# Optimization experiments

Measured on AMD Instinct MI355X. Metric: run time of the kernel, lower is better.

## Reference

```python
import jax, jax.numpy as jnp
import numpy as np

B, T, HH, WW, D, NH, MLPD, KH, KW = 2, 16, 24, 24, 128, 4, 512, 5, 5
T_ = T + 1
HW = HH * WW
SIZE = KH * KW
PH, PW = KH // 2, KW // 2


def _ln(x, w, b):
    m = x.mean(-1, keepdims=True)
    v = ((x - m) ** 2).mean(-1, keepdims=True)
    return (x - m) / jnp.sqrt(v + 1e-5) * w + b


def _mha(q, kv, mask, Wq, bq, Wk, bk, Wv, bv, Wo, bo):
    # q: (N, Lq, D), kv: (N, Lk, D), mask: (N, Lq|1, Lk) True = masked
    N, Lq, Dm = q.shape
    dh = Dm // NH
    qh = (q @ Wq + bq).reshape(N, Lq, NH, dh).transpose(0, 2, 1, 3)
    kh = (kv @ Wk + bk).reshape(N, -1, NH, dh).transpose(0, 2, 1, 3)
    vh = (kv @ Wv + bv).reshape(N, -1, NH, dh).transpose(0, 2, 1, 3)
    scores = jnp.einsum('nhqd,nhkd->nhqk', qh, kh) * (1.0 / np.sqrt(dh))
    logits = jnp.where(mask[:, None, :, :], -1e9, scores)
    attn = jax.nn.softmax(logits, axis=-1)
    out = jnp.einsum('nhqk,nhkd->nhqd', attn, vh).transpose(0, 2, 1, 3).reshape(N, Lq, Dm)
    return out @ Wo + bo, logits


def _unfold_patches(x):
    # x: (N, H, W, D) -> (N, H, W, SIZE, D), kernel positions row-major (matches F.unfold)
    xp = jnp.pad(x, ((0, 0), (PH, PH), (PW, PW), (0, 0)))
    return jnp.stack([xp[:, i:i + HH, j:j + WW, :] for i in range(KH) for j in range(KW)], axis=3)


def setup_inputs() -> dict:
    key = jax.random.key(0)
    ks = iter(jax.random.split(key, 48))
    w = lambda *s: jax.random.normal(next(ks), s, jnp.float32) * 0.02
    inp = {
        'query': jax.random.normal(next(ks), (B, T_, HW, D), jnp.float32),
        'spatial_mask': jnp.zeros((1,), bool),  # ignored by the module
        'temporal_mask': jnp.zeros((B * HW, T_, T_), bool),
        'ln_s_w': jnp.ones((D,), jnp.float32), 'ln_s_b': jnp.zeros((D,), jnp.float32),
        'sWq': w(D, D), 'sbq': jnp.zeros((D,), jnp.float32),
        'sWk': w(D, D), 'sbk': jnp.zeros((D,), jnp.float32),
        'sWv': w(D, D), 'sbv': jnp.zeros((D,), jnp.float32),
        'sWo': w(D, D), 'sbo': jnp.zeros((D,), jnp.float32),
        'ln_t_w': jnp.ones((D,), jnp.float32), 'ln_t_b': jnp.zeros((D,), jnp.float32),
        'tWq': w(D, D), 'tbq': jnp.zeros((D,), jnp.float32),
        'tWk': w(D, D), 'tbk': jnp.zeros((D,), jnp.float32),
        'tWv': w(D, D), 'tbv': jnp.zeros((D,), jnp.float32),
        'tWo': w(D, D), 'tbo': jnp.zeros((D,), jnp.float32),
        'ln_m_w': jnp.ones((D,), jnp.float32), 'ln_m_b': jnp.zeros((D,), jnp.float32),
        'mW1': w(D, MLPD), 'mb1': jnp.zeros((MLPD,), jnp.float32),
        'mW2': w(MLPD, D), 'mb2': jnp.zeros((D,), jnp.float32),
    }
    return inp


def reference(query, spatial_mask, temporal_mask, ln_s_w, ln_s_b, sWq, sbq, sWk, sbk, sWv, sbv, sWo, sbo,
              ln_t_w, ln_t_b, tWq, tbq, tWk, tbk, tWv, tbv, tWo, tbo, ln_m_w, ln_m_b, mW1, mb1, mW2, mb2):
    # ---- spatial branch (local window attention + global CLS key) ----
    visual = query[:, 1:].reshape(B * T, HH, WW, D)
    neigh = _unfold_patches(visual).reshape(B * T * HW, SIZE, D)
    vis = visual.reshape(B * T * HW, 1, D)
    cls = query[:, 0].mean(axis=1, keepdims=True)              # (B,1,D)
    cls_rep = jnp.tile(cls, (T * HW, 1, 1))                    # faithful to torch .repeat ordering
    kv = jnp.concatenate([cls_rep, neigh], axis=1)             # (N, SIZE+1, D)
    # padding mask: True where neighbor falls outside the frame (faithful: CLS zero-col appended LAST)
    valid = jnp.pad(jnp.ones((HH, WW), bool), ((PH, PH), (PW, PW)))
    mpat = jnp.stack([valid[i:i + HH, j:j + WW] for i in range(KH) for j in range(KW)], axis=2).reshape(HW, SIZE)
    smask = jnp.concatenate([~mpat, jnp.zeros((HW, 1), bool)], axis=1)           # (HW, SIZE+1)
    smask = jnp.broadcast_to(smask[None], (B * T, HW, SIZE + 1)).reshape(B * T * HW, 1, SIZE + 1)
    out, _ = _mha(_ln(vis, ln_s_w, ln_s_b), _ln(kv, ln_s_w, ln_s_b), smask,
                  sWq, sbq, sWk, sbk, sWv, sbv, sWo, sbo)
    x = out + vis
    x = jnp.concatenate([query[:, 0:1], x.reshape(B, T, HW, D)], axis=1)  # (B, T_, HW, D)
    # ---- temporal branch ----
    xt = x.transpose(0, 2, 1, 3).reshape(B * HW, T_, D)
    xn = _ln(xt, ln_t_w, ln_t_b)
    x_, logits = _mha(xn, xn, temporal_mask, tWq, tbq, tWk, tbk, tWv, tbv, tWo, tbo)
    xt = x_ + xt
    x = xt.reshape(B, HW, T_, D).transpose(0, 2, 1, 3)
    x = x.at[:, 0].set(x[:, 0:1].mean(axis=2))                 # average CLS across spatial locations
    logits = logits.reshape(B, HW, NH, T_, T_)
    # ---- MLP ----
    h = _ln(x, ln_m_w, ln_m_b)
    h = jax.nn.gelu(h @ mW1 + mb1, approximate=False) @ mW2 + mb2
    x = h + x
    return x, logits
```

## Files before the change

### kernel.cpp

```cpp
#include <hip/hip_runtime.h>
#include <math.h>

#define BB    2
#define TT    16
#define TP    17
#define HH_   24
#define WW_   24
#define HWW   576
#define DD    128
#define NHH   4
#define MLPD_ 512
#define NPIX  18432
#define NTOK  19584
#define SCALE 0.17677669529663688f
#define OUT0_SIZE 2506752

typedef unsigned short u16;
typedef __bf16 bf16x8 __attribute__((ext_vector_type(8)));
typedef float f32x4 __attribute__((ext_vector_type(4)));

__device__ __forceinline__ u16 f2b(float f) {
  unsigned u = __float_as_uint(f);
  u += 0x7FFFu + ((u >> 16) & 1u);
  return (u16)(u >> 16);
}
__device__ __forceinline__ float blo(unsigned u) { return __uint_as_float(u << 16); }
__device__ __forceinline__ float bhi(unsigned u) { return __uint_as_float(u & 0xFFFF0000u); }
__device__ __forceinline__ float b2f(u16 u) { return __uint_as_float((unsigned)u << 16); }

__device__ __forceinline__ float dot8p(uint4 a, uint4 b) {
  float s = blo(a.x) * blo(b.x) + bhi(a.x) * bhi(b.x);
  s += blo(a.y) * blo(b.y) + bhi(a.y) * bhi(b.y);
  s += blo(a.z) * blo(b.z) + bhi(a.z) * bhi(b.z);
  s += blo(a.w) * blo(b.w) + bhi(a.w) * bhi(b.w);
  return s;
}
__device__ __forceinline__ float getp(const float4* P, int j) {
  float4 v = P[j >> 2];
  switch (j & 3) { case 0: return v.x; case 1: return v.y; case 2: return v.z; default: return v.w; }
}
__device__ __forceinline__ void gld_lds16(const void* g, void* l) {
  __builtin_amdgcn_global_load_lds(
      (const __attribute__((address_space(1))) void*)g,
      (__attribute__((address_space(3))) void*)l, 16, 0, 0);
}
__device__ __forceinline__ float fgelu(float x) {
  float u = x * (0.7978845608028654f + 0.03567740814f * x * x);
  u = fminf(fmaxf(u, -15.f), 15.f);
  float e = __expf(2.0f * u);
  return x * e / (e + 1.0f);
}

#define QLN8_BODY(SP, Q8, LNW, LNB, EMIT)                                        \
  {                                                                              \
    const float4* s4_ = (const float4*)(SP) + (Q8) * 4;                          \
    float4 xv_[4];                                                               \
    float sum_ = 0.f, sq_ = 0.f;                                                 \
    _Pragma("unroll")                                                            \
    for (int i_ = 0; i_ < 4; i_++) {                                             \
      float4 a_ = s4_[i_]; xv_[i_] = a_;                                         \
      sum_ += (a_.x + a_.y) + (a_.z + a_.w);                                     \
      sq_  += a_.x * a_.x + a_.y * a_.y + a_.z * a_.z + a_.w * a_.w;             \
    }                                                                            \
    sum_ += __shfl_xor(sum_, 1, 8); sum_ += __shfl_xor(sum_, 2, 8);              \
    sum_ += __shfl_xor(sum_, 4, 8);                                              \
    sq_  += __shfl_xor(sq_, 1, 8);  sq_  += __shfl_xor(sq_, 2, 8);               \
    sq_  += __shfl_xor(sq_, 4, 8);                                               \
    float mean_ = sum_ * (1.0f / DD);                                            \
    float inv_ = rsqrtf(sq_ * (1.0f / DD) - mean_ * mean_ + 1e-5f);              \
    const float4* w4_ = (const float4*)(LNW) + (Q8) * 4;                         \
    const float4* b4_ = (const float4*)(LNB) + (Q8) * 4;                         \
    _Pragma("unroll")                                                            \
    for (int i_ = 0; i_ < 2; i_++) {                                             \
      float4 a0_ = xv_[2 * i_], a1_ = xv_[2 * i_ + 1];                           \
      float4 w0_ = w4_[2 * i_], w1_ = w4_[2 * i_ + 1];                           \
      float4 c0_ = b4_[2 * i_], c1_ = b4_[2 * i_ + 1];                           \
      uint4 o_;                                                                  \
      o_.x = (unsigned)f2b((a0_.x - mean_) * inv_ * w0_.x + c0_.x)               \
           | ((unsigned)f2b((a0_.y - mean_) * inv_ * w0_.y + c0_.y) << 16);      \
      o_.y = (unsigned)f2b((a0_.z - mean_) * inv_ * w0_.z + c0_.z)               \
           | ((unsigned)f2b((a0_.w - mean_) * inv_ * w0_.w + c0_.w) << 16);      \
      o_.z = (unsigned)f2b((a1_.x - mean_) * inv_ * w1_.x + c1_.x)               \
           | ((unsigned)f2b((a1_.y - mean_) * inv_ * w1_.y + c1_.y) << 16);      \
      o_.w = (unsigned)f2b((a1_.z - mean_) * inv_ * w1_.z + c1_.z)               \
           | ((unsigned)f2b((a1_.w - mean_) * inv_ * w1_.w + c1_.w) << 16);      \
      EMIT(i_, o_);                                                              \
    }                                                                            \
  }

#define QLN_BODY(SP, Q, LNW, LNB, EMIT)                                          \
  {                                                                              \
    const float4* s4_ = (const float4*)(SP) + (Q) * 8;                           \
    float4 xv_[8];                                                               \
    float sum_ = 0.f, sq_ = 0.f;                                                 \
    _Pragma("unroll")                                                            \
    for (int i_ = 0; i_ < 8; i_++) {                                             \
      float4 a_ = s4_[i_]; xv_[i_] = a_;                                         \
      sum_ += (a_.x + a_.y) + (a_.z + a_.w);                                     \
      sq_  += a_.x * a_.x + a_.y * a_.y + a_.z * a_.z + a_.w * a_.w;             \
    }                                                                            \
    sum_ += __shfl_xor(sum_, 1, 4); sum_ += __shfl_xor(sum_, 2, 4);              \
    sq_  += __shfl_xor(sq_, 1, 4);  sq_  += __shfl_xor(sq_, 2, 4);               \
    float mean_ = sum_ * (1.0f / DD);                                            \
    float inv_ = rsqrtf(sq_ * (1.0f / DD) - mean_ * mean_ + 1e-5f);              \
    const float4* w4_ = (const float4*)(LNW) + (Q) * 8;                          \
    const float4* b4_ = (const float4*)(LNB) + (Q) * 8;                          \
    _Pragma("unroll")                                                            \
    for (int i_ = 0; i_ < 4; i_++) {                                             \
      float4 a0_ = xv_[2 * i_], a1_ = xv_[2 * i_ + 1];                           \
      float4 w0_ = w4_[2 * i_], w1_ = w4_[2 * i_ + 1];                           \
      float4 c0_ = b4_[2 * i_], c1_ = b4_[2 * i_ + 1];                           \
      uint4 o_;                                                                  \
      o_.x = (unsigned)f2b((a0_.x - mean_) * inv_ * w0_.x + c0_.x)               \
           | ((unsigned)f2b((a0_.y - mean_) * inv_ * w0_.y + c0_.y) << 16);      \
      o_.y = (unsigned)f2b((a0_.z - mean_) * inv_ * w0_.z + c0_.z)               \
           | ((unsigned)f2b((a0_.w - mean_) * inv_ * w0_.w + c0_.w) << 16);      \
      o_.z = (unsigned)f2b((a1_.x - mean_) * inv_ * w1_.x + c1_.x)               \
           | ((unsigned)f2b((a1_.y - mean_) * inv_ * w1_.y + c1_.y) << 16);      \
      o_.w = (unsigned)f2b((a1_.z - mean_) * inv_ * w1_.z + c1_.z)               \
           | ((unsigned)f2b((a1_.w - mean_) * inv_ * w1_.w + c1_.w) << 16);      \
      EMIT(i_, o_);                                                              \
    }                                                                            \
  }

#define MFMA_32x128(ASP, BSP, WR, WC, LANE, ACC)                                 \
  _Pragma("unroll")                                                              \
  for (int kc_ = 0; kc_ < 4; kc_++) {                                            \
    int kob_ = (kc_ * 32 + ((LANE) >> 4) * 8) * 2;                               \
    int ra_ = (WR) * 16 + ((LANE) & 15);                                         \
    bf16x8 af_ = *(const bf16x8*)((const char*)(ASP) + ((ra_ * 256 + kob_) ^ ((ra_ & 7) << 4))); \
    _Pragma("unroll")                                                            \
    for (int j_ = 0; j_ < 4; j_++) {                                             \
      int rb_ = (WC) * 64 + j_ * 16 + ((LANE) & 15);                             \
      bf16x8 bf_ = *(const bf16x8*)((const char*)(BSP) + ((rb_ * 256 + kob_) ^ ((rb_ & 7) << 4))); \
      ACC[j_] = __builtin_amdgcn_mfma_f32_16x16x32_bf16(af_, bf_, ACC[j_], 0, 0, 0); \
    }                                                                            \
  }

__global__ void k_packprep(const float* w0, const float* w1, const float* w2, const float* w3,
                           const float* w4, const float* w5, const float* w6, const float* w7,
                           const float* w8, const float* w9,
                           const float* sbq, const float* sbk, const float* sbv,
                           const float* tbq, const float* tbk, const float* tbv,
                           const float* query, const float* ln_w, const float* ln_b,
                           u16* __restrict__ out, float* __restrict__ sb3, float* __restrict__ tb3,
                           u16* __restrict__ KCb, u16* __restrict__ VCb) {
  int bid = blockIdx.x, tid = threadIdx.x;
  if (bid < 1027) {
    int idx = bid * 256 + tid;
    if (idx < 131072) {
      int seg = idx >> 14, local = idx & 16383;
      const float* tbl[8] = {w0, w1, w2, w3, w4, w5, w6, w7};
      int kk = local >> 7, nn = local & 127;
      out[seg * 16384 + nn * 128 + kk] = f2b(tbl[seg][local]);
    } else if (idx < 196608) {
      int local = idx - 131072;
      int kk = local >> 9, nn = local & 511;
      out[131072 + nn * 128 + kk] = f2b(w8[local]);
    } else if (idx < 262144) {
      int local = idx - 196608;
      int kk = local >> 7, nn = local & 127;
      out[196608 + nn * 512 + kk] = f2b(w9[local]);
    } else if (idx < 262528) {
      int i = idx - 262144;
      sb3[i] = i < 128 ? sbq[i] : (i < 256 ? sbk[i - 128] : sbv[i - 256]);
    } else if (idx < 262912) {
      int i = idx - 262528;
      tb3[i] = i < 128 ? tbq[i] : (i < 256 ? tbk[i - 128] : tbv[i - 256]);
    }
    return;
  }
  __shared__ float part[2][DD];
  __shared__ float xr[DD];
  __shared__ float pk[2][DD], pv[2][DD];
  int r = bid - 1027;
  int c = tid >> 7, d = tid & 127;
  if (r < BB) {
    const float* base = query + (size_t)r * TP * HWW * DD + d;
    float s = 0.f;
    for (int hw = c * 288; hw < c * 288 + 288; ++hw) s += base[(size_t)hw * DD];
    part[c][d] = s;
    __syncthreads();
    if (tid < DD) part[0][tid] = (part[0][tid] + part[1][tid]) * (1.0f / HWW);
    __syncthreads();
    if (tid < DD) {
      float mean = 0.f;
      for (int i = 0; i < DD; i++) mean += part[0][i];
      mean *= (1.0f / DD);
      float var = 0.f;
      for (int i = 0; i < DD; i++) { float t = part[0][i] - mean; var += t * t; }
      var *= (1.0f / DD);
      xr[tid] = (part[0][tid] - mean) * rsqrtf(var + 1e-5f) * ln_w[tid] + ln_b[tid];
    }
  } else {
    if (tid < DD) xr[tid] = ln_b[tid];
  }
  __syncthreads();
  float sk = 0.f, sv = 0.f;
  for (int e = c * 64; e < c * 64 + 64; e++) {
    float xe = xr[e];
    sk += xe * w1[e * DD + d];
    sv += xe * w2[e * DD + d];
  }
  pk[c][d] = sk; pv[c][d] = sv;
  __syncthreads();
  if (tid < DD) {
    float k = pk[0][tid] + pk[1][tid] + sbk[tid];
    float v = pv[0][tid] + pv[1][tid] + sbv[tid];
    KCb[r * DD + tid] = f2b(k);
    VCb[r * DD + tid] = f2b(v);
  }
}

__global__ __launch_bounds__(256, 2) void k_gemm(
    const float* __restrict__ Av, const float* __restrict__ lnw, const float* __restrict__ lnb,
    const u16* __restrict__ Wt, const float* __restrict__ bias,
    u16* __restrict__ Cb, int ldc) {
  __shared__ __align__(16) u16 As[64 * 128];
  __shared__ __align__(16) u16 Bs[128 * 128];
  int tx = threadIdx.x;
  int row0 = blockIdx.x * 64, col0 = blockIdx.y * 128;
  int lane = tx & 63, wid = tx >> 6;
  f32x4 z = {0.f, 0.f, 0.f, 0.f};
  f32x4 acc[2][4];
#pragma unroll
  for (int i = 0; i < 2; i++)
#pragma unroll
    for (int j = 0; j < 4; j++) acc[i][j] = z;

  {
    int rloc = tx >> 2, q = tx & 3;
    int r = row0 + rloc;
    int b2 = r / (TT * HWW); int r2 = r - b2 * (TT * HWW);
    const float* sp = Av + ((size_t)b2 * TP * HWW + HWW + r2) * DD;
#define EMIT_AS(i_, o_) { int dstb = (rloc * 256 + q * 64 + (i_) * 16) ^ ((rloc & 7) << 4); \
                          *(uint4*)((char*)As + dstb) = o_; }
    QLN_BODY(sp, q, lnw, lnb, EMIT_AS)
#undef EMIT_AS
  }
#pragma unroll
  for (int t = 0; t < 8; t++) {
    int ci = t * 256 + tx;
    int r = ci >> 4;
    int c16 = (ci ^ (r & 7)) & 15;
    gld_lds16(&Wt[(size_t)(col0 + r) * 128 + c16 * 8], (char*)Bs + ci * 16);
  }
  __syncthreads();
#pragma unroll
  for (int kc = 0; kc < 4; kc++) {
    int kob = (kc * 32 + (lane >> 4) * 8) * 2;
    bf16x8 af[2], bfr[4];
#pragma unroll
    for (int i = 0; i < 2; i++) {
      int ra = (wid >> 1) * 32 + i * 16 + (lane & 15);
      af[i] = *(const bf16x8*)((const char*)As + ((ra * 256 + kob) ^ ((ra & 7) << 4)));
    }
#pragma unroll
    for (int j = 0; j < 4; j++) {
      int rb = (wid & 1) * 64 + j * 16 + (lane & 15);
      bfr[j] = *(const bf16x8*)((const char*)Bs + ((rb * 256 + kob) ^ ((rb & 7) << 4)));
    }
#pragma unroll
    for (int i = 0; i < 2; i++)
#pragma unroll
      for (int j = 0; j < 4; j++)
        acc[i][j] = __builtin_amdgcn_mfma_f32_16x16x32_bf16(af[i], bfr[j], acc[i][j], 0, 0, 0);
  }

  int rbase = row0 + (wid >> 1) * 32 + (lane >> 4) * 4;
  int cbase = col0 + (wid & 1) * 64 + (lane & 15);
#pragma unroll
  for (int i = 0; i < 2; i++)
#pragma unroll
    for (int e = 0; e < 4; e++) {
      int r = rbase + i * 16 + e;
#pragma unroll
      for (int j = 0; j < 4; j++) {
        int c = cbase + j * 16;
        Cb[(size_t)r * ldc + c] = f2b(acc[i][j][e] + bias[c]);
      }
    }
}

__global__ __launch_bounds__(256, 3) void k_f1(
    const u16* __restrict__ S0b, const float* __restrict__ query,
    const u16* __restrict__ WT, const float* __restrict__ sbo, const float* __restrict__ tb3,
    const float* __restrict__ lnw, const float* __restrict__ lnb,
    float* __restrict__ XB, u16* __restrict__ QKVb) {
  __shared__ __align__(16) char smem[49152];
  u16* As  = (u16*)smem;
  u16* Bs  = (u16*)(smem + 8192);
  float* L = (float*)smem;
  u16* As2 = (u16*)(smem + 40960);
  int tx = threadIdx.x, bid = blockIdx.x;
  int lane = tx & 63, wid = tx >> 6;
  int wr = wid >> 1, wc = wid & 1;
  f32x4 z = {0.f, 0.f, 0.f, 0.f};
  int rb0 = wr * 16 + (lane >> 4) * 4;
  int cb0 = wc * 64 + (lane & 15);
  size_t row0T;

  if (bid < 576) {
    int row0P = bid * 32;
    int b2 = row0P / (TT * HWW);
    row0T = (size_t)row0P + (size_t)(b2 + 1) * HWW;
#pragma unroll
    for (int t = 0; t < 2; t++) {
      int ci = t * 256 + tx; int r = ci >> 4; int c16 = (ci ^ (r & 7)) & 15;
      gld_lds16(&S0b[(size_t)(row0P + r) * 128 + c16 * 8], (char*)As + ci * 16);
    }
    const u16* Wo = WT + 49152;
#pragma unroll
    for (int t = 0; t < 8; t++) {
      int ci = t * 256 + tx; int r = ci >> 4; int c16 = (ci ^ (r & 7)) & 15;
      gld_lds16(&Wo[(size_t)r * 128 + c16 * 8], (char*)Bs + ci * 16);
    }
    __syncthreads();
    f32x4 acc[4];
#pragma unroll
    for (int j = 0; j < 4; j++) acc[j] = z;
    MFMA_32x128(As, Bs, wr, wc, lane, acc)
    __syncthreads();
#pragma unroll
    for (int e = 0; e < 4; e++) {
      int r = rb0 + e;
#pragma unroll
      for (int j = 0; j < 4; j++) {
        int c = cb0 + j * 16;
        float v = acc[j][e] + sbo[c] + query[(row0T + r) * DD + c];
        XB[(row0T + r) * DD + c] = v;
        L[r * 132 + c] = v;
      }
    }
    __syncthreads();
    int rloc = tx >> 3, q8 = tx & 7;
    const float* sp = L + rloc * 132;
#define EMIT_AS2(i_, o_) { int dstb = (rloc * 256 + q8 * 32 + (i_) * 16) ^ ((rloc & 7) << 4); \
                           *(uint4*)((char*)As2 + dstb) = o_; }
    QLN8_BODY(sp, q8, lnw, lnb, EMIT_AS2)
#undef EMIT_AS2
  } else {
    int pb = bid - 576;
    row0T = (size_t)(pb / 18) * TP * HWW + (size_t)(pb % 18) * 32;
    int rloc = tx >> 3, q8 = tx & 7;
    const float* sp = query + (row0T + rloc) * DD;
#define EMIT_AS2(i_, o_) { int dstb = (rloc * 256 + q8 * 32 + (i_) * 16) ^ ((rloc & 7) << 4); \
                           *(uint4*)((char*)As2 + dstb) = o_; }
    QLN8_BODY(sp, q8, lnw, lnb, EMIT_AS2)
#undef EMIT_AS2
  }
  __syncthreads();

  const u16* Wq = WT + 65536;
  for (int by = 0; by < 3; by++) {
    if (by) __syncthreads();
#pragma unroll
    for (int t = 0; t < 8; t++) {
      int ci = t * 256 + tx; int r = ci >> 4; int c16 = (ci ^ (r & 7)) & 15;
      gld_lds16(&Wq[(size_t)(by * 128 + r) * 128 + c16 * 8], (char*)Bs + ci * 16);
    }
    __syncthreads();
    f32x4 acc[4];
#pragma unroll
    for (int j = 0; j < 4; j++) acc[j] = z;
    MFMA_32x128(As2, Bs, wr, wc, lane, acc)
#pragma unroll
    for (int e = 0; e < 4; e++) {
      int r = rb0 + e;
#pragma unroll
      for (int j = 0; j < 4; j++) {
        int c = cb0 + j * 16;
        QKVb[(row0T + r) * 384 + by * 128 + c] = f2b(acc[j][e] + tb3[by * 128 + c]);
      }
    }
  }
}

__global__ __launch_bounds__(256, 3) void k_f2(
    const u16* __restrict__ S0b, const float* __restrict__ XB, const float* __restrict__ query,
    const u16* __restrict__ WT, const float* __restrict__ tbo,
    const float* __restrict__ mb1, const float* __restrict__ mb2,
    const float* __restrict__ lnw, const float* __restrict__ lnb,
    float* __restrict__ X2, float* __restrict__ out0) {
  __shared__ __align__(16) char smem[49152];
  u16* As  = (u16*)smem;
  u16* Bs  = (u16*)(smem + 8192);
  float* L = (float*)smem;
  u16* As2 = (u16*)(smem + 40960);
  u16* Hs  = (u16*)smem;
  int tx = threadIdx.x, bid = blockIdx.x;
  int lane = tx & 63, wid = tx >> 6;
  int wr = wid >> 1, wc = wid & 1;
  bool isV = bid < 576;
  size_t row0T = isV ? ((size_t)(bid / 288) * TP * HWW + HWW + (size_t)(bid % 288) * 32)
                     : ((size_t)((bid - 576) / 18) * TP * HWW + (size_t)((bid - 576) % 18) * 32);
  f32x4 z = {0.f, 0.f, 0.f, 0.f};
  int rb0 = wr * 16 + (lane >> 4) * 4;
  int cb0 = wc * 64 + (lane & 15);

#pragma unroll
  for (int t = 0; t < 2; t++) {
    int ci = t * 256 + tx; int r = ci >> 4; int c16 = (ci ^ (r & 7)) & 15;
    gld_lds16(&S0b[(row0T + r) * 128 + c16 * 8], (char*)As + ci * 16);
  }
  const u16* Wo = WT + 114688;
#pragma unroll
  for (int t = 0; t < 8; t++) {
    int ci = t * 256 + tx; int r = ci >> 4; int c16 = (ci ^ (r & 7)) & 15;
    gld_lds16(&Wo[(size_t)r * 128 + c16 * 8], (char*)Bs + ci * 16);
  }
  __syncthreads();
  f32x4 acc[4];
#pragma unroll
  for (int j = 0; j < 4; j++) acc[j] = z;
  MFMA_32x128(As, Bs, wr, wc, lane, acc)
  __syncthreads();

  f32x4 xres[4];
  const float* res = isV ? XB : query;
#pragma unroll
  for (int e = 0; e < 4; e++) {
    int r = rb0 + e;
#pragma unroll
    for (int j = 0; j < 4; j++) {
      int c = cb0 + j * 16;
      float v = acc[j][e] + tbo[c] + res[(row0T + r) * DD + c];
      xres[j][e] = v;
      if (isV) L[r * 132 + c] = v;
      else     X2[(row0T + r) * DD + c] = v;
    }
  }
  if (!isV) return;
  __syncthreads();
  {
    int rloc = tx >> 3, q8 = tx & 7;
    const float* sp = L + rloc * 132;
#define EMIT_AS2(i_, o_) { int dstb = (rloc * 256 + q8 * 32 + (i_) * 16) ^ ((rloc & 7) << 4); \
                           *(uint4*)((char*)As2 + dstb) = o_; }
    QLN8_BODY(sp, q8, lnw, lnb, EMIT_AS2)
#undef EMIT_AS2
  }
  __syncthreads();

  const u16* W1 = WT + 131072;
  const u16* W2 = WT + 196608;
  f32x4 accC[4];
#pragma unroll
  for (int j = 0; j < 4; j++) accC[j] = z;

  for (int nb = 0; nb < 4; nb++) {
    if (nb) __syncthreads();
#pragma unroll
    for (int t = 0; t < 8; t++) {
      int ci = t * 256 + tx; int r = ci >> 4; int c16 = (ci ^ (r & 7)) & 15;
      gld_lds16(&W1[(size_t)(nb * 128 + r) * 128 + c16 * 8], (char*)Bs + ci * 16);
    }
    __syncthreads();
    f32x4 accH[4];
#pragma unroll
    for (int j = 0; j < 4; j++) accH[j] = z;
    MFMA_32x128(As2, Bs, wr, wc, lane, accH)
    __syncthreads();
#pragma unroll
    for (int e = 0; e < 4; e++) {
      int hr = rb0 + e;
#pragma unroll
      for (int j = 0; j < 4; j++) {
        int hc = cb0 + j * 16;
        float v = fgelu(accH[j][e] + mb1[nb * 128 + hc]);
        *(u16*)((char*)Hs + ((hr * 256 + hc * 2) ^ ((hr & 7) << 4))) = f2b(v);
      }
    }
#pragma unroll
    for (int t = 0; t < 8; t++) {
      int ci = t * 256 + tx; int r = ci >> 4; int c16 = (ci ^ (r & 7)) & 15;
      gld_lds16(&W2[(size_t)r * 512 + nb * 128 + c16 * 8], (char*)Bs + ci * 16);
    }
    __syncthreads();
    MFMA_32x128(Hs, Bs, wr, wc, lane, accC)
  }

#pragma unroll
  for (int e = 0; e < 4; e++) {
    int r = rb0 + e;
#pragma unroll
    for (int j = 0; j < 4; j++) {
      int c = cb0 + j * 16;
      out0[(row0T + r) * DD + c] = accC[j][e] + mb2[c] + xres[j][e];
    }
  }
}

__global__ __launch_bounds__(256) void k_sattn(const u16* __restrict__ qkvb,
                                               const u16* __restrict__ KCb,
                                               const u16* __restrict__ VCb,
                                               u16* __restrict__ outb) {
  __shared__ float Ps[8][32];
  int tid = threadIdx.x;
  int g = tid >> 5, lj = tid & 31;
  int bid = blockIdx.x;
  int blk = (bid & 7) * 1152 + (bid >> 3);
  int G = blk * 8 + g;
  int n = G >> 2, h = G & 3;
  int f = n / HWW, hw = n - f * HWW;
  int hp = hw / WW_, wp = hw - hp * WW_;
  size_t FB = (size_t)f * HWW * 384;

  const u16* kp;
  bool masked;
  if (lj == 0) {
    kp = KCb + (n & 1) * DD + h * 32;
    masked = !(hp >= 2 && wp >= 2);
  } else {
    int k = lj - 1;
    int y = hp + k / 5 - 2, x = wp + k % 5 - 2;
    bool vok = ((unsigned)y < 24u) & ((unsigned)x < 24u) & (k < 25);
    kp = vok ? (qkvb + FB + (size_t)(y * WW_ + x) * 384 + 128 + h * 32)
             : (KCb + BB * DD + h * 32);
    if (lj < 25) { int ym = hp + lj / 5 - 2, xm = wp + lj % 5 - 2;
                   masked = !(((unsigned)ym < 24u) & ((unsigned)xm < 24u)); }
    else masked = false;
  }
  const uint4* q4p = (const uint4*)(qkvb + (size_t)n * 384 + h * 32);
  const uint4* k4p = (const uint4*)kp;
  float s = 0.f;
#pragma unroll
  for (int i = 0; i < 4; i++) s += dot8p(q4p[i], k4p[i]);

  float scr = masked ? -1e9f : s * SCALE;
  if (lj >= 26) scr = -1e30f;
  float mx = scr;
#pragma unroll
  for (int o = 16; o > 0; o >>= 1) mx = fmaxf(mx, __shfl_xor(mx, o, 32));
  float p = __expf(scr - mx);
  float sum = p;
#pragma unroll
  for (int o = 16; o > 0; o >>= 1) sum += __shfl_xor(sum, o, 32);
  Ps[g][lj] = p * (1.0f / sum);

  float4 P4[7];
#pragma unroll
  for (int i = 0; i < 7; i++) P4[i] = *(const float4*)&Ps[g][i * 4];

  float o = getp(P4, 0) * b2f(VCb[(n & 1) * DD + h * 32 + lj]);
#pragma unroll
  for (int k = 0; k < 25; k++) {
    int y = hp + k / 5 - 2, x = wp + k % 5 - 2;
    bool vok = ((unsigned)y < 24u) & ((unsigned)x < 24u);
    const u16* vp = vok ? (qkvb + FB + (size_t)(y * WW_ + x) * 384 + 256)
                        : (VCb + BB * DD);
    o += getp(P4, k + 1) * b2f(vp[h * 32 + lj]);
  }
  outb[(size_t)n * DD + h * 32 + lj] = f2b(o);
}

__global__ __launch_bounds__(256) void k_tattn(const u16* __restrict__ qkv,
                                               u16* __restrict__ outb,
                                               float* __restrict__ logits) {
  __shared__ float Qs[8][TP][32];
  __shared__ float Ps[8][TP][17];
  int tid = threadIdx.x;
  int g = tid >> 5, lj = tid & 31;
  int s = blockIdx.x * 2 + (g >> 2);
  int h = g & 3;
  int b = s / HWW, hw = s - b * HWW;
  size_t base = ((size_t)b * TP * HWW + hw) * 384 + h * 32;
  const size_t TSTR = (size_t)HWW * 384;

  float kreg[32];
  {
    const uint4* k4 = (const uint4*)(qkv + base + (size_t)(lj < 17 ? lj : 16) * TSTR + 128);
#pragma unroll
    for (int i = 0; i < 4; i++) {
      uint4 u = k4[i];
      kreg[i * 8 + 0] = blo(u.x); kreg[i * 8 + 1] = bhi(u.x);
      kreg[i * 8 + 2] = blo(u.y); kreg[i * 8 + 3] = bhi(u.y);
      kreg[i * 8 + 4] = blo(u.z); kreg[i * 8 + 5] = bhi(u.z);
      kreg[i * 8 + 6] = blo(u.w); kreg[i * 8 + 7] = bhi(u.w);
    }
  }
  float vreg[TP];
#pragma unroll
  for (int t = 0; t < TP; t++) {
    Qs[g][t][lj] = b2f(qkv[base + (size_t)t * TSTR + lj]);
    vreg[t]      = b2f(qkv[base + (size_t)t * TSTR + 256 + lj]);
  }

  float* lp = logits + (size_t)s * (NHH * TP * TP) + (size_t)h * (TP * TP);
#pragma unroll 4
  for (int tq = 0; tq < TP; tq++) {
    const float4* qrow = (const float4*)&Qs[g][tq][0];
    float a0 = 0.f, a1 = 0.f, a2 = 0.f, a3 = 0.f;
#pragma unroll
    for (int d4 = 0; d4 < 8; d4++) {
      float4 q4 = qrow[d4];
      a0 += q4.x * kreg[d4 * 4 + 0];
      a1 += q4.y * kreg[d4 * 4 + 1];
      a2 += q4.z * kreg[d4 * 4 + 2];
      a3 += q4.w * kreg[d4 * 4 + 3];
    }
    float sc = ((a0 + a1) + (a2 + a3)) * SCALE;
    if (lj < 17) lp[tq * 17 + lj] = sc;
    float scm = (lj < 17) ? sc : -1e30f;
    float mx = scm;
#pragma unroll
    for (int o = 16; o > 0; o >>= 1) mx = fmaxf(mx, __shfl_xor(mx, o, 32));
    float p = __expf(scm - mx);
    float sum = p;
#pragma unroll
    for (int o = 16; o > 0; o >>= 1) sum += __shfl_xor(sum, o, 32);
    if (lj < 17) Ps[g][tq][lj] = p * (1.0f / sum);
  }
#pragma unroll 4
  for (int tq = 0; tq < TP; tq++) {
    const float* prow = &Ps[g][tq][0];
    float o = 0.f;
#pragma unroll
    for (int t = 0; t < TP; t++) o += prow[t] * vreg[t];
    size_t r = ((size_t)b * TP + tq) * HWW + hw;
    outb[r * DD + h * 32 + lj] = f2b(o);
  }
}

__global__ void k_f3(const float* __restrict__ x2,
                     const float* __restrict__ mW1, const float* __restrict__ mb1,
                     const float* __restrict__ mW2, const float* __restrict__ mb2,
                     const float* __restrict__ lnw, const float* __restrict__ lnb,
                     float* __restrict__ out0) {
  __shared__ float part[4][DD];
  __shared__ float cls[DD];
  __shared__ float lnr[DD];
  __shared__ float H[MLPD_];
  __shared__ float orow[DD];
  int b = blockIdx.x, tid = threadIdx.x;
  int c = tid >> 7, d = tid & 127;
  const float* base = x2 + (size_t)b * TP * HWW * DD;
  float s = 0.f;
  for (int hw = c * 144; hw < c * 144 + 144; ++hw) s += base[(size_t)hw * DD + d];
  part[c][d] = s;
  __syncthreads();
  if (tid < DD) cls[tid] = (part[0][tid] + part[1][tid] + part[2][tid] + part[3][tid]) * (1.0f / HWW);
  __syncthreads();
  if (tid < DD) {
    float mean = 0.f;
    for (int i = 0; i < DD; i++) mean += cls[i];
    mean *= (1.0f / DD);
    float var = 0.f;
    for (int i = 0; i < DD; i++) { float t = cls[i] - mean; var += t * t; }
    var *= (1.0f / DD);
    lnr[tid] = (cls[tid] - mean) * rsqrtf(var + 1e-5f) * lnw[tid] + lnb[tid];
  }
  __syncthreads();
  {
    float a = mb1[tid];
    for (int k = 0; k < DD; k++) a += lnr[k] * mW1[k * MLPD_ + tid];
    H[tid] = 0.5f * a * (1.0f + erff(a * 0.70710678118654752f));
  }
  __syncthreads();
  if (tid < DD) {
    float a = mb2[tid];
    for (int k = 0; k < MLPD_; k++) a += H[k] * mW2[k * DD + tid];
    orow[tid] = a + cls[tid];
  }
  __syncthreads();
  float* ob = out0 + (size_t)b * TP * HWW * DD;
  for (int idx = tid; idx < HWW * DD; idx += 512) ob[idx] = orow[idx & 127];
}

extern "C" void kernel_launch(void* const* d_in, const int* in_sizes, int n_in,
                              void* d_out, int out_size, void* d_ws, size_t ws_size,
                              hipStream_t stream) {
  const float* query  = (const float*)d_in[0];
  const float* ln_s_w = (const float*)d_in[3];
  const float* ln_s_b = (const float*)d_in[4];
  const float* sWq = (const float*)d_in[5];  const float* sbq = (const float*)d_in[6];
  const float* sWk = (const float*)d_in[7];  const float* sbk = (const float*)d_in[8];
  const float* sWv = (const float*)d_in[9];  const float* sbv = (const float*)d_in[10];
  const float* sWo = (const float*)d_in[11]; const float* sbo = (const float*)d_in[12];
  const float* ln_t_w = (const float*)d_in[13];
  const float* ln_t_b = (const float*)d_in[14];
  const float* tWq = (const float*)d_in[15]; const float* tbq = (const float*)d_in[16];
  const float* tWk = (const float*)d_in[17]; const float* tbk = (const float*)d_in[18];
  const float* tWv = (const float*)d_in[19]; const float* tbv = (const float*)d_in[20];
  const float* tWo = (const float*)d_in[21]; const float* tbo = (const float*)d_in[22];
  const float* ln_m_w = (const float*)d_in[23];
  const float* ln_m_b = (const float*)d_in[24];
  const float* mW1 = (const float*)d_in[25]; const float* mb1 = (const float*)d_in[26];
  const float* mW2 = (const float*)d_in[27]; const float* mb2 = (const float*)d_in[28];

  float* ws = (float*)d_ws;
  u16*   QKVb = (u16*)ws;
  u16*   S0b  = (u16*)(ws + 7520256);
  float* XB   = ws + 8773632;
  float* X2   = ws + 11280384;
  u16*   WT   = (u16*)(ws + 13787136);
  float* sb3  = ws + 13918208;
  float* tb3  = ws + 13918592;
  u16*   KCb  = (u16*)(ws + 13920000);
  u16*   VCb  = (u16*)(ws + 13920192);

  float* out0   = (float*)d_out;
  float* logits = out0 + OUT0_SIZE;

  k_packprep<<<1030, 256, 0, stream>>>(sWq, sWk, sWv, sWo, tWq, tWk, tWv, tWo, mW1, mW2,
                                       sbq, sbk, sbv, tbq, tbk, tbv,
                                       query, ln_s_w, ln_s_b, WT, sb3, tb3, KCb, VCb);
  k_gemm<<<dim3(288, 3), 256, 0, stream>>>(query, ln_s_w, ln_s_b, WT, sb3, QKVb, 384);
  k_sattn<<<9216, 256, 0, stream>>>(QKVb, KCb, VCb, S0b);
  k_f1<<<612, 256, 0, stream>>>(S0b, query, WT, sbo, tb3, ln_t_w, ln_t_b, XB, QKVb);
  k_tattn<<<BB * HWW / 2, 256, 0, stream>>>(QKVb, S0b, logits);
  k_f2<<<612, 256, 0, stream>>>(S0b, XB, query, WT, tbo, mb1, mb2, ln_m_w, ln_m_b, X2, out0);
  k_f3<<<2, 512, 0, stream>>>(X2, mW1, mb1, mW2, mb2, ln_m_w, ln_m_b, out0);
}
```

Measured before the change: 156.8 us.

## Fuse temporal attention into output-projection and MLP kernel per spatial pair

Merges the temporal attention kernel into the following Wo projection + LayerNorm + MLP kernel. Each block handles two spatial positions across all 17 timesteps, staging their QKV rows in LDS and keeping the attention output in LDS instead of writing it to global memory and reading it back. The GEMM tiles change to 48 rows (34 valid) with a new MFMA macro, which wastes some MFMA work on padding rows. LDS use grows to 72KB and occupancy drops to 2 blocks per CU.

```diff
diff --git a/kernel.cpp b/kernel.cpp
--- a/kernel.cpp
+++ b/kernel.cpp
@@ -137,6 +137,26 @@
     }                                                                            \
   }
 
+#define MFMA_48x128(ASP, BSP, WID, LANE, ACC)                                    \
+  _Pragma("unroll")                                                              \
+  for (int kc_ = 0; kc_ < 4; kc_++) {                                            \
+    int kob_ = (kc_ * 32 + ((LANE) >> 4) * 8) * 2;                               \
+    bf16x8 bfv_[2];                                                              \
+    _Pragma("unroll")                                                            \
+    for (int j_ = 0; j_ < 2; j_++) {                                             \
+      int rbb_ = (WID) * 32 + j_ * 16 + ((LANE) & 15);                           \
+      bfv_[j_] = *(const bf16x8*)((const char*)(BSP) + ((rbb_ * 256 + kob_) ^ ((rbb_ & 7) << 4))); \
+    }                                                                            \
+    _Pragma("unroll")                                                            \
+    for (int rb_ = 0; rb_ < 3; rb_++) {                                          \
+      int ra_ = rb_ * 16 + ((LANE) & 15);                                        \
+      bf16x8 af_ = *(const bf16x8*)((const char*)(ASP) + ((ra_ * 256 + kob_) ^ ((ra_ & 7) << 4))); \
+      _Pragma("unroll")                                                          \
+      for (int j_ = 0; j_ < 2; j_++)                                             \
+        ACC[rb_][j_] = __builtin_amdgcn_mfma_f32_16x16x32_bf16(af_, bfv_[j_], ACC[rb_][j_], 0, 0, 0); \
+    }                                                                            \
+  }
+
 __global__ void k_packprep(const float* w0, const float* w1, const float* w2, const float* w3,
                            const float* w4, const float* w5, const float* w6, const float* w7,
                            const float* w8, const float* w9,
@@ -376,33 +396,99 @@
   }
 }
 
-__global__ __launch_bounds__(256, 3) void k_f2(
-    const u16* __restrict__ S0b, const float* __restrict__ XB, const float* __restrict__ query,
+__global__ __launch_bounds__(256, 2) void k_f2t(
+    const u16* __restrict__ QKVb, const float* __restrict__ XB, const float* __restrict__ query,
     const u16* __restrict__ WT, const float* __restrict__ tbo,
     const float* __restrict__ mb1, const float* __restrict__ mb2,
     const float* __restrict__ lnw, const float* __restrict__ lnb,
-    float* __restrict__ X2, float* __restrict__ out0) {
-  __shared__ __align__(16) char smem[49152];
-  u16* As  = (u16*)smem;
-  u16* Bs  = (u16*)(smem + 8192);
-  float* L = (float*)smem;
-  u16* As2 = (u16*)(smem + 40960);
-  u16* Hs  = (u16*)smem;
+    float* __restrict__ X2, float* __restrict__ out0, float* __restrict__ logits) {
+  __shared__ __align__(16) char smem[73728];
+  u16* Qkv   = (u16*)smem;
+  u16* atile = (u16*)smem;
+  u16* As2   = (u16*)smem;
+  float* L   = (float*)(smem + 12288);
+  u16* Hs    = (u16*)(smem + 12288);
+  float* Qsf = (float*)(smem + 36864);
+  float* Ps  = (float*)(smem + 54272);
+  u16* Bs    = (u16*)(smem + 40960);
   int tx = threadIdx.x, bid = blockIdx.x;
   int lane = tx & 63, wid = tx >> 6;
-  int wr = wid >> 1, wc = wid & 1;
-  bool isV = bid < 576;
-  size_t row0T = isV ? ((size_t)(bid / 288) * TP * HWW + HWW + (size_t)(bid % 288) * 32)
-                     : ((size_t)((bid - 576) / 18) * TP * HWW + (size_t)((bid - 576) % 18) * 32);
+  int b = bid / 288, hw0 = (bid - b * 288) * 2;
   f32x4 z = {0.f, 0.f, 0.f, 0.f};
-  int rb0 = wr * 16 + (lane >> 4) * 4;
-  int cb0 = wc * 64 + (lane & 15);
-
-#pragma unroll
-  for (int t = 0; t < 2; t++) {
-    int ci = t * 256 + tx; int r = ci >> 4; int c16 = (ci ^ (r & 7)) & 15;
-    gld_lds16(&S0b[(row0T + r) * 128 + c16 * 8], (char*)As + ci * 16);
-  }
+
+#pragma unroll
+  for (int t5 = 0; t5 < 7; t5++) {
+    int ci = t5 * 256 + tx;
+    if (ci < 1632) {
+      int row = ci / 48, c = ci - row * 48;
+      int cp = (c & ~7) | ((c ^ (row & 7)) & 7);
+      int hwi = row / 17, t = row - hwi * 17;
+      size_t tok = (size_t)b * TP * HWW + (size_t)t * HWW + hw0 + hwi;
+      gld_lds16(&QKVb[tok * 384 + cp * 8], (char*)Qkv + ci * 16);
+    }
+  }
+  __syncthreads();
+
+  int g = tx >> 5, lj = tx & 31;
+  int ahwi = g >> 2, ah = g & 3;
+  float kreg[32];
+  {
+    int ro = ahwi * 17 + (lj < 17 ? lj : 16);
+    int base = ro * 768 + 256 + ah * 64, sw = (ro & 7) << 4;
+#pragma unroll
+    for (int i = 0; i < 4; i++) {
+      uint4 u = *(const uint4*)((const char*)Qkv + ((base + i * 16) ^ sw));
+      kreg[i * 8 + 0] = blo(u.x); kreg[i * 8 + 1] = bhi(u.x);
+      kreg[i * 8 + 2] = blo(u.y); kreg[i * 8 + 3] = bhi(u.y);
+      kreg[i * 8 + 4] = blo(u.z); kreg[i * 8 + 5] = bhi(u.z);
+      kreg[i * 8 + 6] = blo(u.w); kreg[i * 8 + 7] = bhi(u.w);
+    }
+  }
+  float vreg[TP];
+#pragma unroll
+  for (int t = 0; t < TP; t++) {
+    int ro = ahwi * 17 + t, sw = (ro & 7) << 4;
+    Qsf[(g * TP + t) * 32 + lj] = b2f(*(const u16*)((const char*)Qkv + ((ro * 768 + (ah * 32 + lj) * 2) ^ sw)));
+    vreg[t] = b2f(*(const u16*)((const char*)Qkv + ((ro * 768 + 512 + ah * 64 + lj * 2) ^ sw)));
+  }
+  __syncthreads();
+
+  float* lp = logits + ((size_t)b * HWW + hw0 + ahwi) * (NHH * TP * TP) + (size_t)ah * (TP * TP);
+#pragma unroll 4
+  for (int tq = 0; tq < TP; tq++) {
+    const float4* qrow = (const float4*)&Qsf[(g * TP + tq) * 32];
+    float a0 = 0.f, a1 = 0.f, a2 = 0.f, a3 = 0.f;
+#pragma unroll
+    for (int d4 = 0; d4 < 8; d4++) {
+      float4 q4 = qrow[d4];
+      a0 += q4.x * kreg[d4 * 4 + 0];
+      a1 += q4.y * kreg[d4 * 4 + 1];
+      a2 += q4.z * kreg[d4 * 4 + 2];
+      a3 += q4.w * kreg[d4 * 4 + 3];
+    }
+    float sc = ((a0 + a1) + (a2 + a3)) * SCALE;
+    if (lj < 17) lp[tq * 17 + lj] = sc;
+    float scm = (lj < 17) ? sc : -1e30f;
+    float mx = scm;
+#pragma unroll
+    for (int o = 16; o > 0; o >>= 1) mx = fmaxf(mx, __shfl_xor(mx, o, 32));
+    float p = __expf(scm - mx);
+    float sum = p;
+#pragma unroll
+    for (int o = 16; o > 0; o >>= 1) sum += __shfl_xor(sum, o, 32);
+    if (lj < 17) Ps[(g * TP + tq) * TP + lj] = p * (1.0f / sum);
+  }
+#pragma unroll 4
+  for (int tq = 0; tq < TP; tq++) {
+    const float* prow = &Ps[(g * TP + tq) * TP];
+    float o = 0.f;
+#pragma unroll
+    for (int t = 0; t < TP; t++) o += prow[t] * vreg[t];
+    int ro = ahwi * 17 + tq;
+    *(u16*)((char*)atile + ((ro * 256 + (ah * 32 + lj) * 2) ^ ((ro & 7) << 4))) = f2b(o);
+  }
+  __syncthreads();
+
   const u16* Wo = WT + 114688;
 #pragma unroll
   for (int t = 0; t < 8; t++) {
@@ -410,43 +496,54 @@
     gld_lds16(&Wo[(size_t)r * 128 + c16 * 8], (char*)Bs + ci * 16);
   }
   __syncthreads();
-  f32x4 acc[4];
-#pragma unroll
-  for (int j = 0; j < 4; j++) acc[j] = z;
-  MFMA_32x128(As, Bs, wr, wc, lane, acc)
-  __syncthreads();
-
-  f32x4 xres[4];
-  const float* res = isV ? XB : query;
-#pragma unroll
-  for (int e = 0; e < 4; e++) {
-    int r = rb0 + e;
-#pragma unroll
-    for (int j = 0; j < 4; j++) {
-      int c = cb0 + j * 16;
-      float v = acc[j][e] + tbo[c] + res[(row0T + r) * DD + c];
-      xres[j][e] = v;
-      if (isV) L[r * 132 + c] = v;
-      else     X2[(row0T + r) * DD + c] = v;
-    }
-  }
-  if (!isV) return;
-  __syncthreads();
+  f32x4 acc1[3][2];
+#pragma unroll
+  for (int i = 0; i < 3; i++)
+#pragma unroll
+    for (int j = 0; j < 2; j++) acc1[i][j] = z;
+  MFMA_48x128(atile, Bs, wid, lane, acc1)
+  __syncthreads();
+
+  f32x4 xres[3][2];
+#pragma unroll
+  for (int rb = 0; rb < 3; rb++)
+#pragma unroll
+    for (int e = 0; e < 4; e++) {
+      int r = rb * 16 + (lane >> 4) * 4 + e;
+      bool valid = r < 34;
+      int hwi2 = r / 17, t2 = r - hwi2 * 17;
+      size_t tok = (size_t)b * TP * HWW + (size_t)t2 * HWW + hw0 + hwi2;
+#pragma unroll
+      for (int j = 0; j < 2; j++) {
+        int c = wid * 32 + j * 16 + (lane & 15);
+        float v = acc1[rb][j][e] + tbo[c];
+        if (valid) v += (t2 == 0 ? query : XB)[tok * DD + c];
+        xres[rb][j][e] = v;
+        if (valid && t2 == 0) X2[tok * DD + c] = v;
+        L[r * 132 + c] = v;
+      }
+    }
+  __syncthreads();
+
   {
-    int rloc = tx >> 3, q8 = tx & 7;
-    const float* sp = L + rloc * 132;
-#define EMIT_AS2(i_, o_) { int dstb = (rloc * 256 + q8 * 32 + (i_) * 16) ^ ((rloc & 7) << 4); \
+    int rloc = tx >> 2, q = tx & 3;
+    if (rloc < 48) {
+      const float* sp = L + rloc * 132;
+#define EMIT_AS2(i_, o_) { int dstb = (rloc * 256 + q * 64 + (i_) * 16) ^ ((rloc & 7) << 4); \
                            *(uint4*)((char*)As2 + dstb) = o_; }
-    QLN8_BODY(sp, q8, lnw, lnb, EMIT_AS2)
+      QLN_BODY(sp, q, lnw, lnb, EMIT_AS2)
 #undef EMIT_AS2
+    }
   }
   __syncthreads();
 
   const u16* W1 = WT + 131072;
   const u16* W2 = WT + 196608;
-  f32x4 accC[4];
-#pragma unroll
-  for (int j = 0; j < 4; j++) accC[j] = z;
+  f32x4 accC[3][2];
+#pragma unroll
+  for (int i = 0; i < 3; i++)
+#pragma unroll
+    for (int j = 0; j < 2; j++) accC[i][j] = z;
 
   for (int nb = 0; nb < 4; nb++) {
     if (nb) __syncthreads();
@@ -456,39 +553,49 @@
       gld_lds16(&W1[(size_t)(nb * 128 + r) * 128 + c16 * 8], (char*)Bs + ci * 16);
     }
     __syncthreads();
-    f32x4 accH[4];
-#pragma unroll
-    for (int j = 0; j < 4; j++) accH[j] = z;
-    MFMA_32x128(As2, Bs, wr, wc, lane, accH)
-    __syncthreads();
-#pragma unroll
-    for (int e = 0; e < 4; e++) {
-      int hr = rb0 + e;
-#pragma unroll
-      for (int j = 0; j < 4; j++) {
-        int hc = cb0 + j * 16;
-        float v = fgelu(accH[j][e] + mb1[nb * 128 + hc]);
-        *(u16*)((char*)Hs + ((hr * 256 + hc * 2) ^ ((hr & 7) << 4))) = f2b(v);
+    f32x4 accH[3][2];
+#pragma unroll
+    for (int i = 0; i < 3; i++)
+#pragma unroll
+      for (int j = 0; j < 2; j++) accH[i][j] = z;
+    MFMA_48x128(As2, Bs, wid, lane, accH)
+    __syncthreads();
+#pragma unroll
+    for (int rb = 0; rb < 3; rb++)
+#pragma unroll
+      for (int e = 0; e < 4; e++) {
+        int hr = rb * 16 + (lane >> 4) * 4 + e;
+#pragma unroll
+        for (int j = 0; j < 2; j++) {
+          int hc = wid * 32 + j * 16 + (lane & 15);
+          float v = fgelu(accH[rb][j][e] + mb1[nb * 128 + hc]);
+          *(u16*)((char*)Hs + ((hr * 256 + hc * 2) ^ ((hr & 7) << 4))) = f2b(v);
+        }
       }
-    }
 #pragma unroll
     for (int t = 0; t < 8; t++) {
       int ci = t * 256 + tx; int r = ci >> 4; int c16 = (ci ^ (r & 7)) & 15;
       gld_lds16(&W2[(size_t)r * 512 + nb * 128 + c16 * 8], (char*)Bs + ci * 16);
     }
     __syncthreads();
-    MFMA_32x128(Hs, Bs, wr, wc, lane, accC)
-  }
-
-#pragma unroll
-  for (int e = 0; e < 4; e++) {
-    int r = rb0 + e;
-#pragma unroll
-    for (int j = 0; j < 4; j++) {
-      int c = cb0 + j * 16;
-      out0[(row0T + r) * DD + c] = accC[j][e] + mb2[c] + xres[j][e];
-    }
-  }
+    MFMA_48x128(Hs, Bs, wid, lane, accC)
+  }
+
+#pragma unroll
+  for (int rb = 0; rb < 3; rb++)
+#pragma unroll
+    for (int e = 0; e < 4; e++) {
+      int r = rb * 16 + (lane >> 4) * 4 + e;
+      if (r >= 34) continue;
+      int hwi2 = r / 17, t2 = r - hwi2 * 17;
+      if (t2 == 0) continue;
+      size_t tok = (size_t)b * TP * HWW + (size_t)t2 * HWW + hw0 + hwi2;
+#pragma unroll
+      for (int j = 0; j < 2; j++) {
+        int c = wid * 32 + j * 16 + (lane & 15);
+        out0[tok * DD + c] = accC[rb][j][e] + mb2[c] + xres[rb][j][e];
+      }
+    }
 }
 
 __global__ __launch_bounds__(256) void k_sattn(const u16* __restrict__ qkvb,
@@ -552,74 +659,6 @@
     o += getp(P4, k + 1) * b2f(vp[h * 32 + lj]);
   }
   outb[(size_t)n * DD + h * 32 + lj] = f2b(o);
-}
-
-__global__ __launch_bounds__(256) void k_tattn(const u16* __restrict__ qkv,
-                                               u16* __restrict__ outb,
-                                               float* __restrict__ logits) {
-  __shared__ float Qs[8][TP][32];
-  __shared__ float Ps[8][TP][17];
-  int tid = threadIdx.x;
-  int g = tid >> 5, lj = tid & 31;
-  int s = blockIdx.x * 2 + (g >> 2);
-  int h = g & 3;
-  int b = s / HWW, hw = s - b * HWW;
-  size_t base = ((size_t)b * TP * HWW + hw) * 384 + h * 32;
-  const size_t TSTR = (size_t)HWW * 384;
-
-  float kreg[32];
-  {
-    const uint4* k4 = (const uint4*)(qkv + base + (size_t)(lj < 17 ? lj : 16) * TSTR + 128);
-#pragma unroll
-    for (int i = 0; i < 4; i++) {
-      uint4 u = k4[i];
-      kreg[i * 8 + 0] = blo(u.x); kreg[i * 8 + 1] = bhi(u.x);
-      kreg[i * 8 + 2] = blo(u.y); kreg[i * 8 + 3] = bhi(u.y);
-      kreg[i * 8 + 4] = blo(u.z); kreg[i * 8 + 5] = bhi(u.z);
-      kreg[i * 8 + 6] = blo(u.w); kreg[i * 8 + 7] = bhi(u.w);
-    }
-  }
-  float vreg[TP];
-#pragma unroll
-  for (int t = 0; t < TP; t++) {
-    Qs[g][t][lj] = b2f(qkv[base + (size_t)t * TSTR + lj]);
-    vreg[t]      = b2f(qkv[base + (size_t)t * TSTR + 256 + lj]);
-  }
-
-  float* lp = logits + (size_t)s * (NHH * TP * TP) + (size_t)h * (TP * TP);
-#pragma unroll 4
-  for (int tq = 0; tq < TP; tq++) {
-    const float4* qrow = (const float4*)&Qs[g][tq][0];
-    float a0 = 0.f, a1 = 0.f, a2 = 0.f, a3 = 0.f;
-#pragma unroll
-    for (int d4 = 0; d4 < 8; d4++) {
-      float4 q4 = qrow[d4];
-      a0 += q4.x * kreg[d4 * 4 + 0];
-      a1 += q4.y * kreg[d4 * 4 + 1];
-      a2 += q4.z * kreg[d4 * 4 + 2];
-      a3 += q4.w * kreg[d4 * 4 + 3];
-    }
-    float sc = ((a0 + a1) + (a2 + a3)) * SCALE;
-    if (lj < 17) lp[tq * 17 + lj] = sc;
-    float scm = (lj < 17) ? sc : -1e30f;
-    float mx = scm;
-#pragma unroll
-    for (int o = 16; o > 0; o >>= 1) mx = fmaxf(mx, __shfl_xor(mx, o, 32));
-    float p = __expf(scm - mx);
-    float sum = p;
-#pragma unroll
-    for (int o = 16; o > 0; o >>= 1) sum += __shfl_xor(sum, o, 32);
-    if (lj < 17) Ps[g][tq][lj] = p * (1.0f / sum);
-  }
-#pragma unroll 4
-  for (int tq = 0; tq < TP; tq++) {
-    const float* prow = &Ps[g][tq][0];
-    float o = 0.f;
-#pragma unroll
-    for (int t = 0; t < TP; t++) o += prow[t] * vreg[t];
-    size_t r = ((size_t)b * TP + tq) * HWW + hw;
-    outb[r * DD + h * 32 + lj] = f2b(o);
-  }
 }
 
 __global__ void k_f3(const float* __restrict__ x2,
@@ -708,7 +747,7 @@
   k_gemm<<<dim3(288, 3), 256, 0, stream>>>(query, ln_s_w, ln_s_b, WT, sb3, QKVb, 384);
   k_sattn<<<9216, 256, 0, stream>>>(QKVb, KCb, VCb, S0b);
   k_f1<<<612, 256, 0, stream>>>(S0b, query, WT, sbo, tb3, ln_t_w, ln_t_b, XB, QKVb);
-  k_tattn<<<BB * HWW / 2, 256, 0, stream>>>(QKVb, S0b, logits);
-  k_f2<<<612, 256, 0, stream>>>(S0b, XB, query, WT, tbo, mb1, mb2, ln_m_w, ln_m_b, X2, out0);
+  k_f2t<<<576, 256, 0, stream>>>(QKVb, XB, query, WT, tbo, mb1, mb2, ln_m_w, ln_m_b,
+                                 X2, out0, logits);
   k_f3<<<2, 512, 0, stream>>>(X2, mW1, mb1, mW2, mb2, ln_m_w, ln_m_b, out0);
 }
```

Result: slower. 174.9 us (+11.5%).

## Compute LayerNorm once per row tile and loop over QKV column blocks

Applied to the files above, without the earlier changes.

The QKV projection kernel previously launched a 288x3 grid in which every column block recomputed the spatial LayerNorm of its 64-row A tile. Now each block takes 32 rows, normalizes them once into shared memory, and loops over the three 128-column weight blocks, reloading only B each time. This removes the triple LayerNorm and the repeated global reads of the input, at the cost of serial B loads inside a block with no overlap. The launch bound is raised to 3 blocks per CU.

```diff
diff --git a/kernel.cpp b/kernel.cpp
--- a/kernel.cpp
+++ b/kernel.cpp
@@ -88,41 +88,6 @@
     }                                                                            \
   }
 
-#define QLN_BODY(SP, Q, LNW, LNB, EMIT)                                          \
-  {                                                                              \
-    const float4* s4_ = (const float4*)(SP) + (Q) * 8;                           \
-    float4 xv_[8];                                                               \
-    float sum_ = 0.f, sq_ = 0.f;                                                 \
-    _Pragma("unroll")                                                            \
-    for (int i_ = 0; i_ < 8; i_++) {                                             \
-      float4 a_ = s4_[i_]; xv_[i_] = a_;                                         \
-      sum_ += (a_.x + a_.y) + (a_.z + a_.w);                                     \
-      sq_  += a_.x * a_.x + a_.y * a_.y + a_.z * a_.z + a_.w * a_.w;             \
-    }                                                                            \
-    sum_ += __shfl_xor(sum_, 1, 4); sum_ += __shfl_xor(sum_, 2, 4);              \
-    sq_  += __shfl_xor(sq_, 1, 4);  sq_  += __shfl_xor(sq_, 2, 4);               \
-    float mean_ = sum_ * (1.0f / DD);                                            \
-    float inv_ = rsqrtf(sq_ * (1.0f / DD) - mean_ * mean_ + 1e-5f);              \
-    const float4* w4_ = (const float4*)(LNW) + (Q) * 8;                          \
-    const float4* b4_ = (const float4*)(LNB) + (Q) * 8;                          \
-    _Pragma("unroll")                                                            \
-    for (int i_ = 0; i_ < 4; i_++) {                                             \
-      float4 a0_ = xv_[2 * i_], a1_ = xv_[2 * i_ + 1];                           \
-      float4 w0_ = w4_[2 * i_], w1_ = w4_[2 * i_ + 1];                           \
-      float4 c0_ = b4_[2 * i_], c1_ = b4_[2 * i_ + 1];                           \
-      uint4 o_;                                                                  \
-      o_.x = (unsigned)f2b((a0_.x - mean_) * inv_ * w0_.x + c0_.x)               \
-           | ((unsigned)f2b((a0_.y - mean_) * inv_ * w0_.y + c0_.y) << 16);      \
-      o_.y = (unsigned)f2b((a0_.z - mean_) * inv_ * w0_.z + c0_.z)               \
-           | ((unsigned)f2b((a0_.w - mean_) * inv_ * w0_.w + c0_.w) << 16);      \
-      o_.z = (unsigned)f2b((a1_.x - mean_) * inv_ * w1_.x + c1_.x)               \
-           | ((unsigned)f2b((a1_.y - mean_) * inv_ * w1_.y + c1_.y) << 16);      \
-      o_.w = (unsigned)f2b((a1_.z - mean_) * inv_ * w1_.z + c1_.z)               \
-           | ((unsigned)f2b((a1_.w - mean_) * inv_ * w1_.w + c1_.w) << 16);      \
-      EMIT(i_, o_);                                                              \
-    }                                                                            \
-  }
-
 #define MFMA_32x128(ASP, BSP, WR, WC, LANE, ACC)                                 \
   _Pragma("unroll")                                                              \
   for (int kc_ = 0; kc_ < 4; kc_++) {                                            \
@@ -212,74 +177,54 @@
   }
 }
 
-__global__ __launch_bounds__(256, 2) void k_gemm(
+__global__ __launch_bounds__(256, 3) void k_gemm(
     const float* __restrict__ Av, const float* __restrict__ lnw, const float* __restrict__ lnb,
-    const u16* __restrict__ Wt, const float* __restrict__ bias,
-    u16* __restrict__ Cb, int ldc) {
-  __shared__ __align__(16) u16 As[64 * 128];
-  __shared__ __align__(16) u16 Bs[128 * 128];
-  int tx = threadIdx.x;
-  int row0 = blockIdx.x * 64, col0 = blockIdx.y * 128;
+    const u16* __restrict__ WT, const float* __restrict__ sb3,
+    u16* __restrict__ Cb) {
+  __shared__ __align__(16) char smem[40960];
+  u16* As = (u16*)smem;
+  u16* Bs = (u16*)(smem + 8192);
+  int tx = threadIdx.x, bid = blockIdx.x;
   int lane = tx & 63, wid = tx >> 6;
+  int wr = wid >> 1, wc = wid & 1;
   f32x4 z = {0.f, 0.f, 0.f, 0.f};
-  f32x4 acc[2][4];
-#pragma unroll
-  for (int i = 0; i < 2; i++)
-#pragma unroll
-    for (int j = 0; j < 4; j++) acc[i][j] = z;
+  int rb0 = wr * 16 + (lane >> 4) * 4;
+  int cb0 = wc * 64 + (lane & 15);
+  int row0 = bid * 32;
 
   {
-    int rloc = tx >> 2, q = tx & 3;
+    int rloc = tx >> 3, q8 = tx & 7;
     int r = row0 + rloc;
     int b2 = r / (TT * HWW); int r2 = r - b2 * (TT * HWW);
     const float* sp = Av + ((size_t)b2 * TP * HWW + HWW + r2) * DD;
-#define EMIT_AS(i_, o_) { int dstb = (rloc * 256 + q * 64 + (i_) * 16) ^ ((rloc & 7) << 4); \
+#define EMIT_AS(i_, o_) { int dstb = (rloc * 256 + q8 * 32 + (i_) * 16) ^ ((rloc & 7) << 4); \
                           *(uint4*)((char*)As + dstb) = o_; }
-    QLN_BODY(sp, q, lnw, lnb, EMIT_AS)
+    QLN8_BODY(sp, q8, lnw, lnb, EMIT_AS)
 #undef EMIT_AS
   }
-#pragma unroll
-  for (int t = 0; t < 8; t++) {
-    int ci = t * 256 + tx;
-    int r = ci >> 4;
-    int c16 = (ci ^ (r & 7)) & 15;
-    gld_lds16(&Wt[(size_t)(col0 + r) * 128 + c16 * 8], (char*)Bs + ci * 16);
-  }
-  __syncthreads();
-#pragma unroll
-  for (int kc = 0; kc < 4; kc++) {
-    int kob = (kc * 32 + (lane >> 4) * 8) * 2;
-    bf16x8 af[2], bfr[4];
-#pragma unroll
-    for (int i = 0; i < 2; i++) {
-      int ra = (wid >> 1) * 32 + i * 16 + (lane & 15);
-      af[i] = *(const bf16x8*)((const char*)As + ((ra * 256 + kob) ^ ((ra & 7) << 4)));
-    }
-#pragma unroll
-    for (int j = 0; j < 4; j++) {
-      int rb = (wid & 1) * 64 + j * 16 + (lane & 15);
-      bfr[j] = *(const bf16x8*)((const char*)Bs + ((rb * 256 + kob) ^ ((rb & 7) << 4)));
-    }
-#pragma unroll
-    for (int i = 0; i < 2; i++)
-#pragma unroll
-      for (int j = 0; j < 4; j++)
-        acc[i][j] = __builtin_amdgcn_mfma_f32_16x16x32_bf16(af[i], bfr[j], acc[i][j], 0, 0, 0);
-  }
-
-  int rbase = row0 + (wid >> 1) * 32 + (lane >> 4) * 4;
-  int cbase = col0 + (wid & 1) * 64 + (lane & 15);
-#pragma unroll
-  for (int i = 0; i < 2; i++)
+
+  for (int by = 0; by < 3; by++) {
+    if (by) __syncthreads();
+#pragma unroll
+    for (int t = 0; t < 8; t++) {
+      int ci = t * 256 + tx; int r = ci >> 4; int c16 = (ci ^ (r & 7)) & 15;
+      gld_lds16(&WT[(size_t)(by * 128 + r) * 128 + c16 * 8], (char*)Bs + ci * 16);
+    }
+    __syncthreads();
+    f32x4 acc[4];
+#pragma unroll
+    for (int j = 0; j < 4; j++) acc[j] = z;
+    MFMA_32x128(As, Bs, wr, wc, lane, acc)
 #pragma unroll
     for (int e = 0; e < 4; e++) {
-      int r = rbase + i * 16 + e;
+      int r = row0 + rb0 + e;
 #pragma unroll
       for (int j = 0; j < 4; j++) {
-        int c = cbase + j * 16;
-        Cb[(size_t)r * ldc + c] = f2b(acc[i][j][e] + bias[c]);
+        int c = cb0 + j * 16;
+        Cb[(size_t)r * 384 + by * 128 + c] = f2b(acc[j][e] + sb3[by * 128 + c]);
       }
     }
+  }
 }
 
 __global__ __launch_bounds__(256, 3) void k_f1(
@@ -705,7 +650,7 @@
   k_packprep<<<1030, 256, 0, stream>>>(sWq, sWk, sWv, sWo, tWq, tWk, tWv, tWo, mW1, mW2,
                                        sbq, sbk, sbv, tbq, tbk, tbv,
                                        query, ln_s_w, ln_s_b, WT, sb3, tb3, KCb, VCb);
-  k_gemm<<<dim3(288, 3), 256, 0, stream>>>(query, ln_s_w, ln_s_b, WT, sb3, QKVb, 384);
+  k_gemm<<<576, 256, 0, stream>>>(query, ln_s_w, ln_s_b, WT, sb3, QKVb);
   k_sattn<<<9216, 256, 0, stream>>>(QKVb, KCb, VCb, S0b);
   k_f1<<<612, 256, 0, stream>>>(S0b, query, WT, sbo, tb3, ln_t_w, ln_t_b, XB, QKVb);
   k_tattn<<<BB * HWW / 2, 256, 0, stream>>>(QKVb, S0b, logits);
```

New measurement: 150.3 us. -4.2%, faster.
